# Kernel tuning notes

Hardware: AMD Instinct MI355X
Metric: run time of the kernel (lower is better)

## Reference

```python
import jax, jax.numpy as jnp
import numpy as np

H, C = 4, 32            # heads, per-head channels (hidden_dim)
F_IN = 128
N_NODES = 50000
N_EDGES = 800000
N_GRAPHS = 64
EPS_SM = 1e-16          # PyG softmax denom eps
EPS_BN = 1e-5


def gat_layer(x, W, a_src, a_dst, b, src, dst, n):
    # x: [N, Fin]; W: [Fin, H*C]; a_src/a_dst: [H, C]; b: [H*C]
    h = (x @ W).reshape(n, H, C)                      # [N,H,C]
    e_src = jnp.einsum('nhc,hc->nh', h, a_src)        # [N,H]
    e_dst = jnp.einsum('nhc,hc->nh', h, a_dst)
    e = jax.nn.leaky_relu(e_src[src] + e_dst[dst], 0.2)  # [E,H]
    m = jax.lax.stop_gradient(jax.ops.segment_max(e, dst, num_segments=n))
    ex = jnp.exp(e - m[dst])
    denom = jax.ops.segment_sum(ex, dst, num_segments=n)
    alpha = ex / (denom[dst] + EPS_SM)                # softmax per destination node
    out = jax.ops.segment_sum(h[src] * alpha[..., None], dst, num_segments=n)
    return out.reshape(n, H * C) + b


def batchnorm(x, gamma, beta):
    # training-mode BN over the node dimension (biased variance)
    mu = x.mean(0)
    var = x.var(0)
    return (x - mu) * jax.lax.rsqrt(var + EPS_BN) * gamma + beta


def setup_inputs() -> dict:
    key = jax.random.key(0)
    ks = jax.random.split(key, 24)
    D = H * C  # 128

    def lin(k, fan_in, shape):
        return jax.random.normal(k, shape, jnp.float32) / np.sqrt(fan_in)

    inp = {
        'x': jax.random.normal(ks[0], (N_NODES, F_IN), jnp.float32),
        'edge_index': jax.random.randint(ks[1], (2, N_EDGES), 0, N_NODES, jnp.int64),
        'node_types': jax.random.randint(ks[2], (N_NODES,), 0, 2, jnp.int64),
        'batch': jnp.sort(jax.random.randint(ks[3], (N_NODES,), 0, N_GRAPHS, jnp.int64)),
        # GAT layer 1 (F_IN -> H*C)
        'W1': lin(ks[4], F_IN, (F_IN, D)), 'as1': lin(ks[5], C, (H, C)),
        'ad1': lin(ks[6], C, (H, C)), 'b1': jnp.zeros((D,), jnp.float32),
        'g1': jnp.ones((D,), jnp.float32), 'be1': jnp.zeros((D,), jnp.float32),
        # GAT layer 2 (D -> D)
        'W2': lin(ks[7], D, (D, D)), 'as2': lin(ks[8], C, (H, C)),
        'ad2': lin(ks[9], C, (H, C)), 'b2': jnp.zeros((D,), jnp.float32),
        'g2': jnp.ones((D,), jnp.float32), 'be2': jnp.zeros((D,), jnp.float32),
        # GAT layer 3 (D -> D)
        'W3': lin(ks[10], D, (D, D)), 'as3': lin(ks[11], C, (H, C)),
        'ad3': lin(ks[12], C, (H, C)), 'b3': jnp.zeros((D,), jnp.float32),
        'g3': jnp.ones((D,), jnp.float32), 'be3': jnp.zeros((D,), jnp.float32),
        # MLP head
        'fc1_w': lin(ks[13], D, (D, C)), 'fc1_b': jnp.zeros((C,), jnp.float32),
        'fc2_w': lin(ks[14], C, (C, 1)), 'fc2_b': jnp.zeros((1,), jnp.float32),
    }
    return inp


def reference(x, edge_index, node_types, batch,
              W1, as1, ad1, b1, g1, be1,
              W2, as2, ad2, b2, g2, be2,
              W3, as3, ad3, b3, g3, be3,
              fc1_w, fc1_b, fc2_w, fc2_b):
    n = x.shape[0]
    # PyG GATConv adds self-loops by default
    loops = jnp.arange(n, dtype=edge_index.dtype)
    src = jnp.concatenate([edge_index[0], loops])
    dst = jnp.concatenate([edge_index[1], loops])
    aw = jnp.where(node_types == 0, 1.5, 1.0).astype(x.dtype)[:, None]  # [N,1]

    h = gat_layer(x, W1, as1, ad1, b1, src, dst, n) * aw
    h = jax.nn.relu(batchnorm(h, g1, be1))
    h = gat_layer(h, W2, as2, ad2, b2, src, dst, n) * aw
    h = jax.nn.relu(batchnorm(h, g2, be2))
    h = gat_layer(h, W3, as3, ad3, b3, src, dst, n) * aw
    h = jax.nn.relu(batchnorm(h, g3, be3))

    # global mean pool over graphs
    sums = jax.ops.segment_sum(h, batch, num_segments=N_GRAPHS)
    cnt = jax.ops.segment_sum(jnp.ones((n,), h.dtype), batch, num_segments=N_GRAPHS)
    pooled = sums / jnp.maximum(cnt, 1.0)[:, None]     # [G, H*C]

    out = jax.nn.relu(pooled @ fc1_w + fc1_b) @ fc2_w + fc2_b  # [G, 1]
    return out
```

## Files before the change

kernel.cpp:

```cpp
#include <hip/hip_runtime.h>
#include <hip/hip_bf16.h>
#include <math.h>

#define NN 50000
#define EE 800000
#define ET_ 850000
#define NG 64
#define NB 196
#define PB 1024
#define GB 391
#define NBK 196
#define BCAP 5120

typedef __attribute__((ext_vector_type(8))) short bf16x8;
typedef __attribute__((ext_vector_type(4))) float f32x4;
typedef __attribute__((ext_vector_type(4))) _Float16 h16x4;

__device__ __forceinline__ void bsplit(float v, ushort& h, ushort& l){
  unsigned u = __float_as_uint(v);
  unsigned hb = (u + 0x7fffu + ((u >> 16) & 1u)) >> 16;
  h = (ushort)hb;
  float hf = __uint_as_float(hb << 16);
  float r = v - hf;
  unsigned ur = __float_as_uint(r);
  l = (ushort)((ur + 0x7fffu + ((ur >> 16) & 1u)) >> 16);
}

__global__ __launch_bounds__(256) void convw(const float* __restrict__ W,
    ushort* __restrict__ wfrag){
  int idx = blockIdx.x*256 + threadIdx.x;
  if (idx >= 128*128) return;
  int c = idx & 127, k = idx >> 7;
  float v = W[idx];
  ushort h, lo;
  bsplit(v, h, lo);
  int dest = (((c>>4)*4 + (k>>5))*64 + (((k&31)>>3)<<4 | (c&15)))*8 + (k&7);
  wfrag[dest] = h;
  wfrag[16384 + dest] = lo;
}

__global__ __launch_bounds__(512) void gemm_fused(const float* __restrict__ X,
    const ushort* __restrict__ wfrag,
    const float* __restrict__ scale, const float* __restrict__ shift,
    const float* __restrict__ av, const float* __restrict__ dv,
    _Float16* __restrict__ H, float* __restrict__ esrc, float* __restrict__ edst, int N){
  __shared__ ushort wl[32768];
  const int tid = threadIdx.x;
  #pragma unroll
  for (int i = 0; i < 8; i++){
    int e = (i*512 + tid) * 8;
    *(bf16x8*)(wl + e) = *(const bf16x8*)(wfrag + e);
  }
  const int w  = tid >> 6;
  const int l  = tid & 63;
  const int lr = l & 15;
  const int lg = l >> 4;
  const int lk = lg * 8;
  const int arow = blockIdx.x*128 + w*16 + lr;
  const bool avl = (arow < N);
  const size_t abase = (size_t)(avl ? arow : 0) * 128;
  bf16x8 ahi[4], alo[4];
  #pragma unroll
  for (int kb = 0; kb < 4; kb++){
    float a[8];
    if (avl){
      *(float4*)(a)   = *(const float4*)(X + abase + kb*32 + lk);
      *(float4*)(a+4) = *(const float4*)(X + abase + kb*32 + lk + 4);
    } else {
      #pragma unroll
      for (int j=0;j<8;j++) a[j] = 0.f;
    }
    if (scale){
      float s[8], b[8];
      *(float4*)(s)   = *(const float4*)(scale + kb*32 + lk);
      *(float4*)(s+4) = *(const float4*)(scale + kb*32 + lk + 4);
      *(float4*)(b)   = *(const float4*)(shift + kb*32 + lk);
      *(float4*)(b+4) = *(const float4*)(shift + kb*32 + lk + 4);
      #pragma unroll
      for (int j=0;j<8;j++) a[j] = fmaxf(fmaf(a[j], s[j], b[j]), 0.f);
    }
    #pragma unroll
    for (int j=0;j<8;j++){
      ushort hh2, ll2;
      bsplit(a[j], hh2, ll2);
      ahi[kb][j] = (short)hh2;
      alo[kb][j] = (short)ll2;
    }
  }
  __syncthreads();
  float esp[4][4], edp[4][4];
  #pragma unroll
  for (int j=0;j<4;j++)
    #pragma unroll
    for (int h=0;h<4;h++){ esp[j][h]=0.f; edp[j][h]=0.f; }
  const int crowb = blockIdx.x*128 + w*16 + lg*4;
  #pragma unroll
  for (int ct = 0; ct < 8; ct++){
    f32x4 acc = {0.f,0.f,0.f,0.f};
    #pragma unroll
    for (int kb = 0; kb < 4; kb++){
      const int fi = ((ct*4 + kb)*64 + l) * 8;
      bf16x8 bhf = *(const bf16x8*)(wl + fi);
      bf16x8 blf = *(const bf16x8*)(wl + 16384 + fi);
      acc = __builtin_amdgcn_mfma_f32_16x16x32_bf16(ahi[kb], bhf, acc, 0, 0, 0);
      acc = __builtin_amdgcn_mfma_f32_16x16x32_bf16(ahi[kb], blf, acc, 0, 0, 0);
      acc = __builtin_amdgcn_mfma_f32_16x16x32_bf16(alo[kb], bhf, acc, 0, 0, 0);
    }
    const int h = ct >> 1;
    const float asv = av[h*32 + (ct&1)*16 + lr];
    const float adv = dv[h*32 + (ct&1)*16 + lr];
    #pragma unroll
    for (int j = 0; j < 4; j++){
      esp[j][h] = fmaf(acc[j], asv, esp[j][h]);
      edp[j][h] = fmaf(acc[j], adv, edp[j][h]);
      int r = crowb + j;
      if (r < N) H[(size_t)r*128 + ct*16 + lr] = (_Float16)acc[j];
    }
  }
  #pragma unroll
  for (int o = 1; o < 16; o <<= 1){
    #pragma unroll
    for (int j=0;j<4;j++)
      #pragma unroll
      for (int h=0;h<4;h++){
        esp[j][h] += __shfl_xor(esp[j][h], o);
        edp[j][h] += __shfl_xor(edp[j][h], o);
      }
  }
  const int jj = lr >> 2, hh = lr & 3;
  float eo = 0.f, dd = 0.f;
  #pragma unroll
  for (int j=0;j<4;j++)
    #pragma unroll
    for (int h=0;h<4;h++){
      bool m = (jj==j) & (hh==h);
      eo = m ? esp[j][h] : eo;
      dd = m ? edp[j][h] : dd;
    }
  const int rw = crowb + jj;
  if (rw < N){
    esrc[rw*4 + hh] = eo;
    edst[rw*4 + hh] = dd;
  }
}

__global__ __launch_bounds__(256) void bin_scatter(const int* __restrict__ ei,
    int* __restrict__ btail, int2* __restrict__ bkt){
  __shared__ int cnt[NBK];
  __shared__ int base[NBK];
  const int t = threadIdx.x;
  for (int i = t; i < NBK; i += 256) cnt[i] = 0;
  __syncthreads();
  int sv[8], dv[8], bv[8], lr[8];
  const int e0 = blockIdx.x*2048;
  #pragma unroll
  for (int k = 0; k < 8; k++){
    int i = e0 + k*256 + t;
    sv[k] = -1;
    if (i < ET_){
      int s, d;
      if (i < EE){ s = ei[i]; d = ei[EE + i]; } else { s = i - EE; d = s; }
      sv[k] = s; dv[k] = d; bv[k] = d >> 8;
      lr[k] = atomicAdd(&cnt[bv[k]], 1);
    }
  }
  __syncthreads();
  for (int i = t; i < NBK; i += 256){
    int c = cnt[i];
    base[i] = c ? atomicAdd(&btail[i], c) : 0;
  }
  __syncthreads();
  #pragma unroll
  for (int k = 0; k < 8; k++){
    if (sv[k] >= 0){
      int p = base[bv[k]] + lr[k];
      if (p < BCAP) bkt[bv[k]*BCAP + p] = make_int2(sv[k], dv[k]);
    }
  }
}

__global__ __launch_bounds__(256) void bucket_count(const int* __restrict__ btail,
    const int2* __restrict__ bkt, int* __restrict__ cnt){
  __shared__ int c256[256];
  const int b = blockIdx.x, t = threadIdx.x;
  c256[t] = 0; __syncthreads();
  int n = btail[b]; if (n > BCAP) n = BCAP;
  for (int i = t; i < n; i += 256){
    int d = bkt[b*BCAP + i].y;
    atomicAdd(&c256[d & 255], 1);
  }
  __syncthreads();
  int node = b*256 + t;
  if (node < NN) cnt[node] = c256[t];
}

__global__ __launch_bounds__(256) void scan_partial(const int* __restrict__ cnt,
    int* __restrict__ rowptr, int* __restrict__ bsum){
  __shared__ int sh[256];
  const int t = threadIdx.x;
  const int i = blockIdx.x*256 + t;
  int v = (i < NN) ? cnt[i] : 0;
  sh[t] = v; __syncthreads();
  for (int o=1;o<256;o<<=1){
    int u = (t>=o) ? sh[t-o] : 0;
    __syncthreads();
    sh[t] += u;
    __syncthreads();
  }
  if (i < NN) rowptr[i] = sh[t] - v;
  if (t == 255) bsum[blockIdx.x] = sh[255];
}

__global__ __launch_bounds__(256) void scan_bsum(int* __restrict__ bsum){
  __shared__ int sh[256];
  const int t = threadIdx.x;
  int v = (t < NB) ? bsum[t] : 0;
  sh[t] = v; __syncthreads();
  for (int o=1;o<256;o<<=1){
    int u = (t>=o) ? sh[t-o] : 0;
    __syncthreads();
    sh[t] += u;
    __syncthreads();
  }
  if (t < NB) bsum[t] = sh[t] - v;
}

__global__ __launch_bounds__(256) void scan_add(int* __restrict__ rowptr,
    const int* __restrict__ bsum){
  const int i = blockIdx.x*256 + threadIdx.x;
  if (i < NN) rowptr[i] += bsum[blockIdx.x];
  if (i == NN) rowptr[NN] = ET_;
}

__global__ __launch_bounds__(256) void bucket_scatter(const int* __restrict__ btail,
    const int2* __restrict__ bkt, const int* __restrict__ rowptr,
    int* __restrict__ csr_src){
  __shared__ int h256[256];
  const int b = blockIdx.x, t = threadIdx.x;
  int node = b*256 + t;
  h256[t] = (node < NN) ? rowptr[node] : 0;
  __syncthreads();
  int n = btail[b]; if (n > BCAP) n = BCAP;
  for (int i = t; i < n; i += 256){
    int2 e = bkt[b*BCAP + i];
    int pos = atomicAdd(&h256[e.y & 255], 1);
    csr_src[pos] = e.x;
  }
}

__global__ __launch_bounds__(256) void gat_fused(const int* __restrict__ rowptr,
    const int* __restrict__ csr_src, const float* __restrict__ esrc,
    const float* __restrict__ edst, const _Float16* __restrict__ hbuf,
    const float* __restrict__ bias, const int* __restrict__ ntype,
    float* __restrict__ y){
  __shared__ int2 pk[4][64][4];
  const int w    = threadIdx.x >> 6;
  const int lane = threadIdx.x & 63;
  const int wid  = blockIdx.x*4 + w;
  if (wid >= NN) return;
  const int d = wid;
  const int beg = rowptr[d], end = rowptr[d+1];
  const float4 ed4 = *(const float4*)(edst + (size_t)d*4);

  const int c4   = (lane & 31) * 4;
  const int eh   = lane >> 5;
  const int head = (lane & 31) >> 3;

  float dn0=0.f, dn1=0.f, dn2=0.f, dn3=0.f;
  float4 acc0 = make_float4(0.f,0.f,0.f,0.f);
  float4 acc1 = make_float4(0.f,0.f,0.f,0.f);

  const int2* pp = &pk[w][eh][head];

  for (int j0 = beg; j0 < end; j0 += 64){
    int j = j0 + lane;
    int s = d;
    float ex0=0.f, ex1=0.f, ex2=0.f, ex3=0.f;
    if (j < end){
      s = csr_src[j];
      float4 es = *(const float4*)(esrc + (size_t)s*4);
      float e0 = es.x + ed4.x; e0 = (e0 > 0.f) ? e0 : 0.2f*e0;
      float e1 = es.y + ed4.y; e1 = (e1 > 0.f) ? e1 : 0.2f*e1;
      float e2 = es.z + ed4.z; e2 = (e2 > 0.f) ? e2 : 0.2f*e2;
      float e3 = es.w + ed4.w; e3 = (e3 > 0.f) ? e3 : 0.2f*e3;
      ex0 = expf(e0); ex1 = expf(e1); ex2 = expf(e2); ex3 = expf(e3);
      dn0 += ex0; dn1 += ex1; dn2 += ex2; dn3 += ex3;
    }
    int4 w0 = make_int4(s, __float_as_int(ex0), s, __float_as_int(ex1));
    int4 w1 = make_int4(s, __float_as_int(ex2), s, __float_as_int(ex3));
    *(int4*)&pk[w][lane][0] = w0;
    *(int4*)&pk[w][lane][2] = w1;
    int cnt2 = end - j0; if (cnt2 > 64) cnt2 = 64;
    const int npair = (cnt2 + 1) >> 1;
    int p = 0;
    #pragma unroll 2
    for (; p + 2 <= npair; p += 2){
      int2 va = pp[p*8];
      int2 vb = pp[p*8 + 8];
      float wa = __int_as_float(va.y);
      float wb = __int_as_float(vb.y);
      h16x4 ha = *(const h16x4*)(hbuf + (size_t)va.x*128 + c4);
      h16x4 hb = *(const h16x4*)(hbuf + (size_t)vb.x*128 + c4);
      acc0.x = fmaf((float)ha.x, wa, acc0.x);
      acc0.y = fmaf((float)ha.y, wa, acc0.y);
      acc0.z = fmaf((float)ha.z, wa, acc0.z);
      acc0.w = fmaf((float)ha.w, wa, acc0.w);
      acc1.x = fmaf((float)hb.x, wb, acc1.x);
      acc1.y = fmaf((float)hb.y, wb, acc1.y);
      acc1.z = fmaf((float)hb.z, wb, acc1.z);
      acc1.w = fmaf((float)hb.w, wb, acc1.w);
    }
    if (p < npair){
      int2 va = pp[p*8];
      float wa = __int_as_float(va.y);
      h16x4 ha = *(const h16x4*)(hbuf + (size_t)va.x*128 + c4);
      acc0.x = fmaf((float)ha.x, wa, acc0.x);
      acc0.y = fmaf((float)ha.y, wa, acc0.y);
      acc0.z = fmaf((float)ha.z, wa, acc0.z);
      acc0.w = fmaf((float)ha.w, wa, acc0.w);
    }
  }
  #pragma unroll
  for (int o = 32; o; o >>= 1){
    dn0 += __shfl_xor(dn0, o);
    dn1 += __shfl_xor(dn1, o);
    dn2 += __shfl_xor(dn2, o);
    dn3 += __shfl_xor(dn3, o);
  }
  float dsel = (head==0) ? dn0 : (head==1) ? dn1 : (head==2) ? dn2 : dn3;
  float inv = 1.f / (dsel + 1e-16f);
  float4 acc;
  acc.x = acc0.x + acc1.x;
  acc.y = acc0.y + acc1.y;
  acc.z = acc0.z + acc1.z;
  acc.w = acc0.w + acc1.w;
  acc.x += __shfl_xor(acc.x, 32);
  acc.y += __shfl_xor(acc.y, 32);
  acc.z += __shfl_xor(acc.z, 32);
  acc.w += __shfl_xor(acc.w, 32);
  if (eh == 0){
    float aw = (ntype[d] == 0) ? 1.5f : 1.0f;
    float4 bb = *(const float4*)(bias + c4);
    float4 o4;
    o4.x = (acc.x*inv + bb.x) * aw;
    o4.y = (acc.y*inv + bb.y) * aw;
    o4.z = (acc.z*inv + bb.z) * aw;
    o4.w = (acc.w*inv + bb.w) * aw;
    *(float4*)(y + (size_t)d*128 + c4) = o4;
  }
}

__global__ __launch_bounds__(256) void epi_stats(const float* __restrict__ y,
    double* __restrict__ bnsum, double* __restrict__ bnsumsq, int N){
  __shared__ float red[256][8];
  const int t = threadIdx.x;
  const int c4 = (t & 31) * 4;
  const int rowInBlk = t >> 5;
  const int stride = gridDim.x * 8;
  float s0=0,s1=0,s2=0,s3=0,q0=0,q1=0,q2=0,q3=0;
  for (int n = blockIdx.x*8 + rowInBlk; n < N; n += stride){
    float4 v = *(const float4*)(y + (size_t)n*128 + c4);
    s0+=v.x; s1+=v.y; s2+=v.z; s3+=v.w;
    q0+=v.x*v.x; q1+=v.y*v.y; q2+=v.z*v.z; q3+=v.w*v.w;
  }
  red[t][0]=s0; red[t][1]=s1; red[t][2]=s2; red[t][3]=s3;
  red[t][4]=q0; red[t][5]=q1; red[t][6]=q2; red[t][7]=q3;
  __syncthreads();
  if (t < 32){
    float a[8] = {0,0,0,0,0,0,0,0};
    for (int j=0;j<8;j++){
      #pragma unroll
      for (int k2=0;k2<8;k2++) a[k2] += red[j*32+t][k2];
    }
    atomicAdd(bnsum   + t*4+0, (double)a[0]);
    atomicAdd(bnsum   + t*4+1, (double)a[1]);
    atomicAdd(bnsum   + t*4+2, (double)a[2]);
    atomicAdd(bnsum   + t*4+3, (double)a[3]);
    atomicAdd(bnsumsq + t*4+0, (double)a[4]);
    atomicAdd(bnsumsq + t*4+1, (double)a[5]);
    atomicAdd(bnsumsq + t*4+2, (double)a[6]);
    atomicAdd(bnsumsq + t*4+3, (double)a[7]);
  }
}

__global__ void bn_final(const double* __restrict__ bnsum, const double* __restrict__ bnsumsq,
    const float* __restrict__ gma, const float* __restrict__ bta,
    float* __restrict__ scale, float* __restrict__ shift, int N){
  int c = threadIdx.x;
  double mu  = bnsum[c] / N;
  double var = bnsumsq[c] / N - mu*mu;
  if (var < 0.0) var = 0.0;
  float inv = (float)(1.0 / sqrt(var + 1e-5));
  float sc  = inv * gma[c];
  scale[c] = sc;
  shift[c] = bta[c] - (float)mu * sc;
}

__global__ __launch_bounds__(256) void pool_partial(const float* __restrict__ y,
    const int* __restrict__ batch, const float* __restrict__ scale,
    const float* __restrict__ shift, float* __restrict__ pooled){
  const int t = threadIdx.x;
  const int c = t & 127;
  const int sub = t >> 7;
  const int per = (NN + PB - 1) / PB;
  const int n0 = blockIdx.x * per;
  int n1 = n0 + per; if (n1 > NN) n1 = NN;
  const float sc = scale[c], sh = shift[c];
  float acc = 0.f;
  int curg = -1;
  for (int n = n0 + sub; n < n1; n += 2){
    int g = batch[n];
    if (g != curg){
      if (curg >= 0) unsafeAtomicAdd(pooled + (size_t)curg*128 + c, acc);
      curg = g; acc = 0.f;
    }
    float v = y[(size_t)n*128 + c];
    acc += fmaxf(fmaf(v, sc, sh), 0.f);
  }
  if (curg >= 0) unsafeAtomicAdd(pooled + (size_t)curg*128 + c, acc);
}

__global__ __launch_bounds__(128) void mlp_head(const float* __restrict__ pooled,
    const int* __restrict__ batch, const float* __restrict__ fc1w,
    const float* __restrict__ fc1b, const float* __restrict__ fc2w,
    const float* __restrict__ fc2b, float* __restrict__ out){
  __shared__ float psh[128];
  __shared__ float hid[32];
  const int g = blockIdx.x, t = threadIdx.x;
  int lo = 0, hi = NN;
  while (lo < hi){ int mid = (lo+hi)>>1; if (batch[mid] < g) lo = mid+1; else hi = mid; }
  const int beg = lo;
  lo = beg; hi = NN;
  while (lo < hi){ int mid = (lo+hi)>>1; if (batch[mid] < g+1) lo = mid+1; else hi = mid; }
  int cntn = lo - beg; if (cntn < 1) cntn = 1;
  psh[t] = pooled[(size_t)g*128 + t] / (float)cntn;
  __syncthreads();
  if (t < 32){
    float a = fc1b[t];
    for (int k=0;k<128;k++) a += psh[k]*fc1w[k*32+t];
    a = (a > 0.f) ? a : 0.f;
    hid[t] = a * fc2w[t];
  }
  __syncthreads();
  if (t == 0){
    float sacc = fc2b[0];
    #pragma unroll
    for (int j=0;j<32;j++) sacc += hid[j];
    out[g] = sacc;
  }
}

extern "C" void kernel_launch(void* const* d_in, const int* in_sizes, int n_in,
                              void* d_out, int out_size, void* d_ws, size_t ws_size,
                              hipStream_t stream){
  const float* x     = (const float*)d_in[0];
  const int*   ei    = (const int*)d_in[1];
  const int*   ntype = (const int*)d_in[2];
  const int*   batch = (const int*)d_in[3];
  const float* Wl[3]  = {(const float*)d_in[4],  (const float*)d_in[10], (const float*)d_in[16]};
  const float* asl[3] = {(const float*)d_in[5],  (const float*)d_in[11], (const float*)d_in[17]};
  const float* adl[3] = {(const float*)d_in[6],  (const float*)d_in[12], (const float*)d_in[18]};
  const float* bl[3]  = {(const float*)d_in[7],  (const float*)d_in[13], (const float*)d_in[19]};
  const float* gl[3]  = {(const float*)d_in[8],  (const float*)d_in[14], (const float*)d_in[20]};
  const float* bel[3] = {(const float*)d_in[9],  (const float*)d_in[15], (const float*)d_in[21]};
  const float* fc1w = (const float*)d_in[22];
  const float* fc1b = (const float*)d_in[23];
  const float* fc2w = (const float*)d_in[24];
  const float* fc2b = (const float*)d_in[25];

  char* base = (char*)d_ws;
  size_t off = 0;
  auto alloc = [&](size_t bytes)->char*{
    size_t o = (off + 255) & ~(size_t)255; off = o + bytes; return base + o;
  };
  _Float16* hbuf = (_Float16*)alloc((size_t)NN*128*2);
  float* y       = (float*)alloc((size_t)NN*128*4);
  ushort* wfrag  = (ushort*)alloc((size_t)32768*2);
  float* esrc    = (float*)alloc((size_t)NN*4*4);
  float* edst    = (float*)alloc((size_t)NN*4*4);
  int*   cnt     = (int*)  alloc((size_t)NN*4);
  int*   rowptr  = (int*)  alloc((size_t)(NN+1)*4);
  int*   csr_src = (int*)  alloc((size_t)ET_*4);
  int*   btail   = (int*)  alloc((size_t)NBK*4);
  int2*  bkt     = (int2*) alloc((size_t)NBK*BCAP*8);
  int*   bsum    = (int*)  alloc((size_t)NB*4);
  double* bnsum  = (double*)alloc(128*8);
  double* bnsumsq= (double*)alloc(128*8);
  float* scale   = (float*)alloc(128*4);
  float* shift   = (float*)alloc(128*4);
  float* pooled  = (float*)alloc((size_t)NG*128*4);
  if (off > ws_size) return;

  hipMemsetAsync(btail, 0, (size_t)NBK*4, stream);
  hipMemsetAsync(pooled, 0, (size_t)NG*128*4, stream);
  bin_scatter<<<(ET_+2047)/2048, 256, 0, stream>>>(ei, btail, bkt);
  bucket_count<<<NBK, 256, 0, stream>>>(btail, bkt, cnt);
  scan_partial<<<NB, 256, 0, stream>>>(cnt, rowptr, bsum);
  scan_bsum<<<1, 256, 0, stream>>>(bsum);
  scan_add<<<NB, 256, 0, stream>>>(rowptr, bsum);
  bucket_scatter<<<NBK, 256, 0, stream>>>(btail, bkt, rowptr, csr_src);

  for (int l = 0; l < 3; l++){
    const float* in = (l==0) ? x : y;
    const float* scl = (l==0) ? nullptr : scale;
    const float* shf = (l==0) ? nullptr : shift;
    hipMemsetAsync(bnsum, 0, 128*8*2, stream);
    convw<<<64, 256, 0, stream>>>(Wl[l], wfrag);
    gemm_fused<<<GB, 512, 0, stream>>>(in, wfrag, scl, shf, asl[l], adl[l],
                                       hbuf, esrc, edst, NN);
    gat_fused<<<(NN+3)/4, 256, 0, stream>>>(rowptr, csr_src, esrc, edst, hbuf, bl[l], ntype, y);
    epi_stats<<<256, 256, 0, stream>>>(y, bnsum, bnsumsq, NN);
    bn_final<<<1, 128, 0, stream>>>(bnsum, bnsumsq, gl[l], bel[l], scale, shift, NN);
  }
  pool_partial<<<PB, 256, 0, stream>>>(y, batch, scale, shift, pooled);
  mlp_head<<<NG, 128, 0, stream>>>(pooled, batch, fc1w, fc1b, fc2w, fc2b, (float*)d_out);
}
```

Measured before the change: 442.7 us.

## Fuse BN statistics into GAT aggregation and compute attention logits via folded MFMA

The GAT aggregation kernel becomes grid-strided over a fixed number of blocks and accumulates per-channel batchnorm sum and sum-of-squares while writing y. Per-block partials are then reduced by a small kernel, which removes the separate pass that re-read the full y array. Separately, the attention vectors are folded into W (W·a_src, W·a_dst) and packed as an extra MFMA B-fragment, so e_src/e_dst come from one extra MFMA tile instead of FMA plus shuffle reductions. The costs are an extra tiny kernel per layer, a change in summation order for the logits, and fewer resident blocks for the gather kernel.

New measurement: 435.2 us. Within noise of the previous version (-1.7%).

```diff
diff --git a/kernel.cpp b/kernel.cpp
--- a/kernel.cpp
+++ b/kernel.cpp
@@ -11,6 +11,7 @@
 #define GB 391
 #define NBK 196
 #define BCAP 5120
+#define GATB 2048
 
 typedef __attribute__((ext_vector_type(8))) short bf16x8;
 typedef __attribute__((ext_vector_type(4))) float f32x4;
@@ -39,10 +40,35 @@
   wfrag[16384 + dest] = lo;
 }
 
+__global__ __launch_bounds__(256) void convea(const float* __restrict__ W,
+    const float* __restrict__ as_, const float* __restrict__ ad_,
+    ushort* __restrict__ eafrag){
+  const int t = threadIdx.x;
+  const int kb = t >> 6, l = t & 63;
+  const int col = l & 15, krow = (l >> 4) * 8;
+  #pragma unroll
+  for (int j = 0; j < 8; j++){
+    int k = kb*32 + krow + j;
+    float v = 0.f;
+    if (col < 8){
+      int h = col & 3;
+      const float* a  = (col < 4) ? (as_ + h*32) : (ad_ + h*32);
+      const float* wr = W + (size_t)k*128 + h*32;
+      float acc = 0.f;
+      #pragma unroll
+      for (int c = 0; c < 32; c++) acc += wr[c]*a[c];
+      v = acc;
+    }
+    ushort hi, lo;
+    bsplit(v, hi, lo);
+    eafrag[(kb*64 + l)*8 + j] = hi;
+    eafrag[2048 + (kb*64 + l)*8 + j] = lo;
+  }
+}
+
 __global__ __launch_bounds__(512) void gemm_fused(const float* __restrict__ X,
-    const ushort* __restrict__ wfrag,
+    const ushort* __restrict__ wfrag, const ushort* __restrict__ eafrag,
     const float* __restrict__ scale, const float* __restrict__ shift,
-    const float* __restrict__ av, const float* __restrict__ dv,
     _Float16* __restrict__ H, float* __restrict__ esrc, float* __restrict__ edst, int N){
   __shared__ ushort wl[32768];
   const int tid = threadIdx.x;
@@ -88,11 +114,6 @@
     }
   }
   __syncthreads();
-  float esp[4][4], edp[4][4];
-  #pragma unroll
-  for (int j=0;j<4;j++)
-    #pragma unroll
-    for (int h=0;h<4;h++){ esp[j][h]=0.f; edp[j][h]=0.f; }
   const int crowb = blockIdx.x*128 + w*16 + lg*4;
   #pragma unroll
   for (int ct = 0; ct < 8; ct++){
@@ -106,41 +127,32 @@
       acc = __builtin_amdgcn_mfma_f32_16x16x32_bf16(ahi[kb], blf, acc, 0, 0, 0);
       acc = __builtin_amdgcn_mfma_f32_16x16x32_bf16(alo[kb], bhf, acc, 0, 0, 0);
     }
-    const int h = ct >> 1;
-    const float asv = av[h*32 + (ct&1)*16 + lr];
-    const float adv = dv[h*32 + (ct&1)*16 + lr];
     #pragma unroll
     for (int j = 0; j < 4; j++){
-      esp[j][h] = fmaf(acc[j], asv, esp[j][h]);
-      edp[j][h] = fmaf(acc[j], adv, edp[j][h]);
       int r = crowb + j;
       if (r < N) H[(size_t)r*128 + ct*16 + lr] = (_Float16)acc[j];
     }
   }
-  #pragma unroll
-  for (int o = 1; o < 16; o <<= 1){
+  {
+    f32x4 acc = {0.f,0.f,0.f,0.f};
     #pragma unroll
-    for (int j=0;j<4;j++)
+    for (int kb = 0; kb < 4; kb++){
+      bf16x8 bhf = *(const bf16x8*)(eafrag + (kb*64 + l)*8);
+      bf16x8 blf = *(const bf16x8*)(eafrag + 2048 + (kb*64 + l)*8);
+      acc = __builtin_amdgcn_mfma_f32_16x16x32_bf16(ahi[kb], bhf, acc, 0, 0, 0);
+      acc = __builtin_amdgcn_mfma_f32_16x16x32_bf16(ahi[kb], blf, acc, 0, 0, 0);
+      acc = __builtin_amdgcn_mfma_f32_16x16x32_bf16(alo[kb], bhf, acc, 0, 0, 0);
+    }
+    if (lr < 8){
       #pragma unroll
-      for (int h=0;h<4;h++){
-        esp[j][h] += __shfl_xor(esp[j][h], o);
-        edp[j][h] += __shfl_xor(edp[j][h], o);
+      for (int j = 0; j < 4; j++){
+        int r = crowb + j;
+        if (r < N){
+          if (lr < 4) esrc[r*4 + lr] = acc[j];
+          else        edst[r*4 + lr - 4] = acc[j];
+        }
       }
-  }
-  const int jj = lr >> 2, hh = lr & 3;
-  float eo = 0.f, dd = 0.f;
-  #pragma unroll
-  for (int j=0;j<4;j++)
-    #pragma unroll
-    for (int h=0;h<4;h++){
-      bool m = (jj==j) & (hh==h);
-      eo = m ? esp[j][h] : eo;
-      dd = m ? edp[j][h] : dd;
-    }
-  const int rw = crowb + jj;
-  if (rw < N){
-    esrc[rw*4 + hh] = eo;
-    edst[rw*4 + hh] = dd;
+    }
   }
 }
 
@@ -252,135 +264,130 @@
     const int* __restrict__ csr_src, const float* __restrict__ esrc,
     const float* __restrict__ edst, const _Float16* __restrict__ hbuf,
     const float* __restrict__ bias, const int* __restrict__ ntype,
-    float* __restrict__ y){
+    float* __restrict__ y, float* __restrict__ bnpart){
   __shared__ int2 pk[4][64][4];
   const int w    = threadIdx.x >> 6;
   const int lane = threadIdx.x & 63;
-  const int wid  = blockIdx.x*4 + w;
-  if (wid >= NN) return;
-  const int d = wid;
-  const int beg = rowptr[d], end = rowptr[d+1];
-  const float4 ed4 = *(const float4*)(edst + (size_t)d*4);
-
   const int c4   = (lane & 31) * 4;
   const int eh   = lane >> 5;
   const int head = (lane & 31) >> 3;
-
-  float dn0=0.f, dn1=0.f, dn2=0.f, dn3=0.f;
-  float4 acc0 = make_float4(0.f,0.f,0.f,0.f);
-  float4 acc1 = make_float4(0.f,0.f,0.f,0.f);
-
   const int2* pp = &pk[w][eh][head];
 
-  for (int j0 = beg; j0 < end; j0 += 64){
-    int j = j0 + lane;
-    int s = d;
-    float ex0=0.f, ex1=0.f, ex2=0.f, ex3=0.f;
-    if (j < end){
-      s = csr_src[j];
-      float4 es = *(const float4*)(esrc + (size_t)s*4);
-      float e0 = es.x + ed4.x; e0 = (e0 > 0.f) ? e0 : 0.2f*e0;
-      float e1 = es.y + ed4.y; e1 = (e1 > 0.f) ? e1 : 0.2f*e1;
-      float e2 = es.z + ed4.z; e2 = (e2 > 0.f) ? e2 : 0.2f*e2;
-      float e3 = es.w + ed4.w; e3 = (e3 > 0.f) ? e3 : 0.2f*e3;
-      ex0 = expf(e0); ex1 = expf(e1); ex2 = expf(e2); ex3 = expf(e3);
-      dn0 += ex0; dn1 += ex1; dn2 += ex2; dn3 += ex3;
-    }
-    int4 w0 = make_int4(s, __float_as_int(ex0), s, __float_as_int(ex1));
-    int4 w1 = make_int4(s, __float_as_int(ex2), s, __float_as_int(ex3));
-    *(int4*)&pk[w][lane][0] = w0;
-    *(int4*)&pk[w][lane][2] = w1;
-    int cnt2 = end - j0; if (cnt2 > 64) cnt2 = 64;
-    const int npair = (cnt2 + 1) >> 1;
-    int p = 0;
-    #pragma unroll 2
-    for (; p + 2 <= npair; p += 2){
-      int2 va = pp[p*8];
-      int2 vb = pp[p*8 + 8];
-      float wa = __int_as_float(va.y);
-      float wb = __int_as_float(vb.y);
-      h16x4 ha = *(const h16x4*)(hbuf + (size_t)va.x*128 + c4);
-      h16x4 hb = *(const h16x4*)(hbuf + (size_t)vb.x*128 + c4);
-      acc0.x = fmaf((float)ha.x, wa, acc0.x);
-      acc0.y = fmaf((float)ha.y, wa, acc0.y);
-      acc0.z = fmaf((float)ha.z, wa, acc0.z);
-      acc0.w = fmaf((float)ha.w, wa, acc0.w);
-      acc1.x = fmaf((float)hb.x, wb, acc1.x);
-      acc1.y = fmaf((float)hb.y, wb, acc1.y);
-      acc1.z = fmaf((float)hb.z, wb, acc1.z);
-      acc1.w = fmaf((float)hb.w, wb, acc1.w);
-    }
-    if (p < npair){
-      int2 va = pp[p*8];
-      float wa = __int_as_float(va.y);
-      h16x4 ha = *(const h16x4*)(hbuf + (size_t)va.x*128 + c4);
-      acc0.x = fmaf((float)ha.x, wa, acc0.x);
-      acc0.y = fmaf((float)ha.y, wa, acc0.y);
-      acc0.z = fmaf((float)ha.z, wa, acc0.z);
-      acc0.w = fmaf((float)ha.w, wa, acc0.w);
-    }
-  }
-  #pragma unroll
-  for (int o = 32; o; o >>= 1){
-    dn0 += __shfl_xor(dn0, o);
-    dn1 += __shfl_xor(dn1, o);
-    dn2 += __shfl_xor(dn2, o);
-    dn3 += __shfl_xor(dn3, o);
-  }
-  float dsel = (head==0) ? dn0 : (head==1) ? dn1 : (head==2) ? dn2 : dn3;
-  float inv = 1.f / (dsel + 1e-16f);
-  float4 acc;
-  acc.x = acc0.x + acc1.x;
-  acc.y = acc0.y + acc1.y;
-  acc.z = acc0.z + acc1.z;
-  acc.w = acc0.w + acc1.w;
-  acc.x += __shfl_xor(acc.x, 32);
-  acc.y += __shfl_xor(acc.y, 32);
-  acc.z += __shfl_xor(acc.z, 32);
-  acc.w += __shfl_xor(acc.w, 32);
+  float bs0=0.f,bs1=0.f,bs2=0.f,bs3=0.f,bq0=0.f,bq1=0.f,bq2=0.f,bq3=0.f;
+  const float4 bb = *(const float4*)(bias + c4);
+
+  for (int d = blockIdx.x*4 + w; d < NN; d += GATB*4){
+    const int beg = rowptr[d], end = rowptr[d+1];
+    const float4 ed4 = *(const float4*)(edst + (size_t)d*4);
+    float dn0=0.f, dn1=0.f, dn2=0.f, dn3=0.f;
+    float4 acc0 = make_float4(0.f,0.f,0.f,0.f);
+    float4 acc1 = make_float4(0.f,0.f,0.f,0.f);
+
+    for (int j0 = beg; j0 < end; j0 += 64){
+      int j = j0 + lane;
+      int s = d;
+      float ex0=0.f, ex1=0.f, ex2=0.f, ex3=0.f;
+      if (j < end){
+        s = csr_src[j];
+        float4 es = *(const float4*)(esrc + (size_t)s*4);
+        float e0 = es.x + ed4.x; e0 = (e0 > 0.f) ? e0 : 0.2f*e0;
+        float e1 = es.y + ed4.y; e1 = (e1 > 0.f) ? e1 : 0.2f*e1;
+        float e2 = es.z + ed4.z; e2 = (e2 > 0.f) ? e2 : 0.2f*e2;
+        float e3 = es.w + ed4.w; e3 = (e3 > 0.f) ? e3 : 0.2f*e3;
+        ex0 = expf(e0); ex1 = expf(e1); ex2 = expf(e2); ex3 = expf(e3);
+        dn0 += ex0; dn1 += ex1; dn2 += ex2; dn3 += ex3;
+      }
+      int4 w0 = make_int4(s, __float_as_int(ex0), s, __float_as_int(ex1));
+      int4 w1 = make_int4(s, __float_as_int(ex2), s, __float_as_int(ex3));
+      *(int4*)&pk[w][lane][0] = w0;
+      *(int4*)&pk[w][lane][2] = w1;
+      int cnt2 = end - j0; if (cnt2 > 64) cnt2 = 64;
+      const int npair = (cnt2 + 1) >> 1;
+      int p = 0;
+      #pragma unroll 2
+      for (; p + 2 <= npair; p += 2){
+        int2 va = pp[p*8];
+        int2 vb = pp[p*8 + 8];
+        float wa = __int_as_float(va.y);
+        float wb = __int_as_float(vb.y);
+        h16x4 ha = *(const h16x4*)(hbuf + (size_t)va.x*128 + c4);
+        h16x4 hb = *(const h16x4*)(hbuf + (size_t)vb.x*128 + c4);
+        acc0.x = fmaf((float)ha.x, wa, acc0.x);
+        acc0.y = fmaf((float)ha.y, wa, acc0.y);
+        acc0.z = fmaf((float)ha.z, wa, acc0.z);
+        acc0.w = fmaf((float)ha.w, wa, acc0.w);
+        acc1.x = fmaf((float)hb.x, wb, acc1.x);
+        acc1.y = fmaf((float)hb.y, wb, acc1.y);
+        acc1.z = fmaf((float)hb.z, wb, acc1.z);
+        acc1.w = fmaf((float)hb.w, wb, acc1.w);
+      }
+      if (p < npair){
+        int2 va = pp[p*8];
+        float wa = __int_as_float(va.y);
+        h16x4 ha = *(const h16x4*)(hbuf + (size_t)va.x*128 + c4);
+        acc0.x = fmaf((float)ha.x, wa, acc0.x);
+        acc0.y = fmaf((float)ha.y, wa, acc0.y);
+        acc0.z = fmaf((float)ha.z, wa, acc0.z);
+        acc0.w = fmaf((float)ha.w, wa, acc0.w);
+      }
+    }
+    #pragma unroll
+    for (int o = 32; o; o >>= 1){
+      dn0 += __shfl_xor(dn0, o);
+      dn1 += __shfl_xor(dn1, o);
+      dn2 += __shfl_xor(dn2, o);
+      dn3 += __shfl_xor(dn3, o);
+    }
+    float dsel = (head==0) ? dn0 : (head==1) ? dn1 : (head==2) ? dn2 : dn3;
+    float inv = 1.f / (dsel + 1e-16f);
+    float4 acc;
+    acc.x = acc0.x + acc1.x;
+    acc.y = acc0.y + acc1.y;
+    acc.z = acc0.z + acc1.z;
+    acc.w = acc0.w + acc1.w;
+    acc.x += __shfl_xor(acc.x, 32);
+    acc.y += __shfl_xor(acc.y, 32);
+    acc.z += __shfl_xor(acc.z, 32);
+    acc.w += __shfl_xor(acc.w, 32);
+    if (eh == 0){
+      float aw = (ntype[d] == 0) ? 1.5f : 1.0f;
+      float4 o4;
+      o4.x = (acc.x*inv + bb.x) * aw;
+      o4.y = (acc.y*inv + bb.y) * aw;
+      o4.z = (acc.z*inv + bb.z) * aw;
+      o4.w = (acc.w*inv + bb.w) * aw;
+      *(float4*)(y + (size_t)d*128 + c4) = o4;
+      bs0 += o4.x; bs1 += o4.y; bs2 += o4.z; bs3 += o4.w;
+      bq0 += o4.x*o4.x; bq1 += o4.y*o4.y; bq2 += o4.z*o4.z; bq3 += o4.w*o4.w;
+    }
+  }
+  __syncthreads();
+  float* bnp = (float*)pk;
   if (eh == 0){
-    float aw = (ntype[d] == 0) ? 1.5f : 1.0f;
-    float4 bb = *(const float4*)(bias + c4);
-    float4 o4;
-    o4.x = (acc.x*inv + bb.x) * aw;
-    o4.y = (acc.y*inv + bb.y) * aw;
-    o4.z = (acc.z*inv + bb.z) * aw;
-    o4.w = (acc.w*inv + bb.w) * aw;
-    *(float4*)(y + (size_t)d*128 + c4) = o4;
-  }
-}
-
-__global__ __launch_bounds__(256) void epi_stats(const float* __restrict__ y,
-    double* __restrict__ bnsum, double* __restrict__ bnsumsq, int N){
-  __shared__ float red[256][8];
+    float* q = bnp + (w*32 + (lane & 31))*8;
+    q[0]=bs0; q[1]=bs1; q[2]=bs2; q[3]=bs3;
+    q[4]=bq0; q[5]=bq1; q[6]=bq2; q[7]=bq3;
+  }
+  __syncthreads();
   const int t = threadIdx.x;
-  const int c4 = (t & 31) * 4;
-  const int rowInBlk = t >> 5;
-  const int stride = gridDim.x * 8;
-  float s0=0,s1=0,s2=0,s3=0,q0=0,q1=0,q2=0,q3=0;
-  for (int n = blockIdx.x*8 + rowInBlk; n < N; n += stride){
-    float4 v = *(const float4*)(y + (size_t)n*128 + c4);
-    s0+=v.x; s1+=v.y; s2+=v.z; s3+=v.w;
-    q0+=v.x*v.x; q1+=v.y*v.y; q2+=v.z*v.z; q3+=v.w*v.w;
-  }
-  red[t][0]=s0; red[t][1]=s1; red[t][2]=s2; red[t][3]=s3;
-  red[t][4]=q0; red[t][5]=q1; red[t][6]=q2; red[t][7]=q3;
-  __syncthreads();
-  if (t < 32){
-    float a[8] = {0,0,0,0,0,0,0,0};
-    for (int j=0;j<8;j++){
-      #pragma unroll
-      for (int k2=0;k2<8;k2++) a[k2] += red[j*32+t][k2];
-    }
-    atomicAdd(bnsum   + t*4+0, (double)a[0]);
-    atomicAdd(bnsum   + t*4+1, (double)a[1]);
-    atomicAdd(bnsum   + t*4+2, (double)a[2]);
-    atomicAdd(bnsum   + t*4+3, (double)a[3]);
-    atomicAdd(bnsumsq + t*4+0, (double)a[4]);
-    atomicAdd(bnsumsq + t*4+1, (double)a[5]);
-    atomicAdd(bnsumsq + t*4+2, (double)a[6]);
-    atomicAdd(bnsumsq + t*4+3, (double)a[7]);
-  }
+  const int c = t & 127, stat = t >> 7;
+  float v = 0.f;
+  #pragma unroll
+  for (int ww = 0; ww < 4; ww++)
+    v += bnp[(ww*32 + (c>>2))*8 + stat*4 + (c&3)];
+  bnpart[(size_t)blockIdx.x*256 + t] = v;
+}
+
+__global__ __launch_bounds__(256) void bn_reduce(const float* __restrict__ bnpart,
+    double* __restrict__ bnsum, double* __restrict__ bnsumsq){
+  const int t = threadIdx.x, b = blockIdx.x;
+  float acc = 0.f;
+  #pragma unroll 4
+  for (int j = 0; j < GATB/64; j++)
+    acc += bnpart[(size_t)(b*(GATB/64) + j)*256 + t];
+  const int c = t & 127;
+  if (t < 128) atomicAdd(bnsum + c, (double)acc);
+  else         atomicAdd(bnsumsq + c, (double)acc);
 }
 
 __global__ void bn_final(const double* __restrict__ bnsum, const double* __restrict__ bnsumsq,
@@ -476,6 +483,7 @@
   _Float16* hbuf = (_Float16*)alloc((size_t)NN*128*2);
   float* y       = (float*)alloc((size_t)NN*128*4);
   ushort* wfrag  = (ushort*)alloc((size_t)32768*2);
+  ushort* eafrag = (ushort*)alloc((size_t)4096*2);
   float* esrc    = (float*)alloc((size_t)NN*4*4);
   float* edst    = (float*)alloc((size_t)NN*4*4);
   int*   cnt     = (int*)  alloc((size_t)NN*4);
@@ -484,6 +492,7 @@
   int*   btail   = (int*)  alloc((size_t)NBK*4);
   int2*  bkt     = (int2*) alloc((size_t)NBK*BCAP*8);
   int*   bsum    = (int*)  alloc((size_t)NB*4);
+  float* bnpart  = (float*)alloc((size_t)GATB*256*4);
   double* bnsum  = (double*)alloc(128*8);
   double* bnsumsq= (double*)alloc(128*8);
   float* scale   = (float*)alloc(128*4);
@@ -506,10 +515,12 @@
     const float* shf = (l==0) ? nullptr : shift;
     hipMemsetAsync(bnsum, 0, 128*8*2, stream);
     convw<<<64, 256, 0, stream>>>(Wl[l], wfrag);
-    gemm_fused<<<GB, 512, 0, stream>>>(in, wfrag, scl, shf, asl[l], adl[l],
+    convea<<<1, 256, 0, stream>>>(Wl[l], asl[l], adl[l], eafrag);
+    gemm_fused<<<GB, 512, 0, stream>>>(in, wfrag, eafrag, scl, shf,
                                        hbuf, esrc, edst, NN);
-    gat_fused<<<(NN+3)/4, 256, 0, stream>>>(rowptr, csr_src, esrc, edst, hbuf, bl[l], ntype, y);
-    epi_stats<<<256, 256, 0, stream>>>(y, bnsum, bnsumsq, NN);
+    gat_fused<<<GATB, 256, 0, stream>>>(rowptr, csr_src, esrc, edst, hbuf,
+                                        bl[l], ntype, y, bnpart);
+    bn_reduce<<<64, 256, 0, stream>>>(bnpart, bnsum, bnsumsq);
     bn_final<<<1, 128, 0, stream>>>(bnsum, bnsumsq, gl[l], bel[l], scale, shift, NN);
   }
   pool_partial<<<PB, 256, 0, stream>>>(y, batch, scale, shift, pooled);
```
